# Kernel tuning notes

Hardware: AMD Instinct MI355X
Metric: run time of the kernel (lower is better)

## Reference

```python
import jax, jax.numpy as jnp
import numpy as np

HEADS = 8

def _flatten(x, s1, s2):
    # 'b c (h s1) (w s2) -> b (h w) (s1 s2 c)'
    b, c, H, W = x.shape
    h, w = H // s1, W // s2
    x = x.reshape(b, c, h, s1, w, s2).transpose(0, 2, 4, 3, 5, 1)
    return x.reshape(b, h * w, s1 * s2 * c)

def _unflatten(x, h, w, s1, s2):
    # 'b (h w) (s1 s2 c) -> b c (h s1) (w s2)'
    b, n, e = x.shape
    c = e // (s1 * s2)
    x = x.reshape(b, h, w, s1, s2, c).transpose(0, 5, 1, 3, 2, 4)
    return x.reshape(b, c, h * s1, w * s2)

def _attn(x_detail, x_context, wq, bq, wk, bk, wv, bv, wo, bo):
    E = x_detail.shape[-1]
    d = E // HEADS
    scale = d ** -0.5
    def split(t):
        b, n, _ = t.shape
        return t.reshape(b, n, HEADS, d).transpose(0, 2, 1, 3)  # b h n d
    q = split(x_context @ wq.T + bq)
    k = split(x_detail @ wk.T + bk)
    v = split(x_detail @ wv.T + bv)
    att = jax.nn.softmax(jnp.einsum('bhqd,bhkd->bhqk', q, k) * scale, axis=-1)
    out = jnp.einsum('bhqk,bhkd->bhqd', att, v)
    b, h, n, _ = out.shape
    out = out.transpose(0, 2, 1, 3).reshape(b, n, E)
    return out @ wo.T + bo

def setup_inputs() -> dict:
    key = jax.random.key(0)
    ks = iter(jax.random.split(key, 64))
    inp = {}
    xshapes = [(16, 96, 56, 56), (16, 192, 28, 28), (16, 384, 14, 14), (16, 768, 7, 7)]
    names = ['x00', 'x10', 'x20', 'x30']
    for nm, sh in zip(names, xshapes):
        inp[nm + '_detail'] = jax.random.normal(next(ks), sh, dtype=jnp.float32)
        inp[nm + '_context'] = jax.random.normal(next(ks), sh, dtype=jnp.float32)
    embs = [384, 192, 384, 768]
    for i, E in enumerate(embs):
        for p in ['q', 'k', 'v', 'o']:
            inp[f'w{p}{i}'] = jax.random.normal(next(ks), (E, E), dtype=jnp.float32) * 0.02
            inp[f'b{p}{i}'] = jnp.zeros((E,), dtype=jnp.float32)
    return inp

def reference(x00_detail, x00_context, x10_detail, x10_context,
              x20_detail, x20_context, x30_detail, x30_context,
              wq0, bq0, wk0, bk0, wv0, bv0, wo0, bo0,
              wq1, bq1, wk1, bk1, wv1, bv1, wo1, bo1,
              wq2, bq2, wk2, bk2, wv2, bv2, wo2, bo2,
              wq3, bq3, wk3, bk3, wv3, bv3, wo3, bo3):
    # scale 0: 56x56 with 2x2 patching -> 784 tokens, emb 384
    o0 = x00_detail + _unflatten(
        _attn(_flatten(x00_detail, 2, 2), _flatten(x00_context, 2, 2),
              wq0, bq0, wk0, bk0, wv0, bv0, wo0, bo0), 28, 28, 2, 2)
    # scale 1: 28x28 -> 784 tokens, emb 192
    o1 = x10_detail + _unflatten(
        _attn(_flatten(x10_detail, 1, 1), _flatten(x10_context, 1, 1),
              wq1, bq1, wk1, bk1, wv1, bv1, wo1, bo1), 28, 28, 1, 1)
    # scale 2: 14x14 -> 196 tokens, emb 384
    o2 = x20_detail + _unflatten(
        _attn(_flatten(x20_detail, 1, 1), _flatten(x20_context, 1, 1),
              wq2, bq2, wk2, bk2, wv2, bv2, wo2, bo2), 14, 14, 1, 1)
    # scale 3: 7x7 -> 49 tokens, emb 768
    o3 = x30_detail + _unflatten(
        _attn(_flatten(x30_detail, 1, 1), _flatten(x30_context, 1, 1),
              wq3, bq3, wk3, bk3, wv3, bv3, wo3, bo3), 7, 7, 1, 1)
    return (o0, o1, o2, o3)
```

## Files before the change

### kernel.cpp

```cpp
#include <hip/hip_runtime.h>
#include <hip/hip_bf16.h>
#include <cstdint>
#include <cstddef>
#include <cmath>

typedef unsigned short bf16u;
typedef float f32x4 __attribute__((ext_vector_type(4)));
typedef short frag8 __attribute__((ext_vector_type(8)));

typedef __attribute__((address_space(1))) uint32_t u32g;
typedef __attribute__((address_space(3))) uint32_t u32l;

__device__ __forceinline__ void async_cp16(const bf16u* g, bf16u* l) {
    __builtin_amdgcn_global_load_lds((u32g*)g, (u32l*)l, 16, 0, 0);
}

__device__ __forceinline__ bf16u f2bf(float f) {
    union { float f; uint32_t u; } v; v.f = f;
    uint32_t u = v.u;
    return (bf16u)((u + 0x7fffu + ((u >> 16) & 1u)) >> 16);
}

__device__ __forceinline__ uint32_t pk2bf(float a, float b) {
    __hip_bfloat162 h = __float22bfloat162_rn(make_float2(a, b));
    union { __hip_bfloat162 h; uint32_t u; } c; c.h = h; return c.u;
}

__device__ __forceinline__ int vperm(int n) {
    return (n & ~63) | ((n & 15) << 2) | ((n >> 4) & 3);
}

static constexpr int cN[4]   = {784, 784, 196, 49};
static constexpr int cE[4]   = {384, 192, 384, 768};
static constexpr int cM[4]   = {12544, 12544, 3136, 784};
static constexpr int cC[4]   = {96, 192, 384, 768};
static constexpr int cH[4]   = {56, 28, 14, 7};
static constexpr int cS[4]   = {2, 1, 1, 1};
static constexpr int cWt[4]  = {28, 28, 14, 7};

static constexpr size_t xoff[4] = {0, 4816896, 7225344, 8429568};
static constexpr size_t voff[4] = {0, 6815744, 10223616, 12320768};
static constexpr size_t woff[4] = {0, 589824, 737280, 1327104};

__device__ __constant__ float qsc[4] = {0.20823509f, 0.29448888f, 0.20823509f, 0.14724444f};

static constexpr int qStartQ[5] = {0, 294, 369, 411, 999};
static constexpr int oStart[5]  = {0,294,369,411,999};

static constexpr int fStart[9] = {0,4800,9600,12000,14400,15744,17088,17856,18624};
static constexpr int wCum[17]  = {0,72,144,216,288,306,324,342,360,432,504,576,648,936,1224,1512,1800};
static constexpr int fNtn[4] = {25, 25, 7, 2};
static constexpr int fNtc[4] = {3, 6, 12, 24};
static constexpr int fSp[4]  = {4, 1, 1, 1};

struct BiasP { const float* p[16]; };
struct PrepP { const float* x[8]; const float* w[16]; };
struct OunfP { const float* xd[4]; };

__global__ __launch_bounds__(256) void prep(PrepP pp, bf16u* __restrict__ Xd,
                                            bf16u* __restrict__ Xc, bf16u* __restrict__ Wb) {
    int blk = blockIdx.x, tid = threadIdx.x;
    if (blk < 18624) {
        __shared__ float tile[32][33];
        int seg = 0;
        while (seg < 7 && blk >= fStart[seg + 1]) seg++;
        int s = seg >> 1, which = seg & 1;
        int l = blk - fStart[seg];
        int ntn = fNtn[s], ntc = fNtc[s], sp = fSp[s];
        int nt = l % ntn; l /= ntn;
        int ctl = l % ntc; l /= ntc;
        int spi = l % sp; int b = l / sp;
        int sv = cS[s];
        int s1i = spi / sv, s2i = spi % sv;
        int C = cC[s], H = cH[s], Wd = cH[s], N = cN[s], E2 = cE[s], Wt = cWt[s];
        const float* x = pp.x[s * 2 + which];
        bf16u* dst = (which ? Xc : Xd) + xoff[s];
        int tx = tid & 31, ty = tid >> 5;
        int n0 = nt * 32, c0 = ctl * 32;
#pragma unroll
        for (int rr = 0; rr < 4; ++rr) {
            int c = c0 + rr * 8 + ty;
            int n = n0 + tx;
            if (n < N) {
                int hh = (n / Wt) * sv + s1i;
                int ww = (n % Wt) * sv + s2i;
                tile[rr * 8 + ty][tx] = x[((size_t)(b * C + c) * H + hh) * Wd + ww];
            }
        }
        __syncthreads();
        int ebase = (s1i * sv + s2i) * C + c0;
#pragma unroll
        for (int rr = 0; rr < 4; ++rr) {
            int n = n0 + rr * 8 + ty;
            if (n < N)
                dst[((size_t)b * N + n) * E2 + ebase + tx] = f2bf(tile[tx][rr * 8 + ty]);
        }
    } else {
        int wb = blk - 18624;
        int m2 = 0;
        while (m2 < 15 && wb >= wCum[m2 + 1]) m2++;
        int s = m2 >> 2, mi = m2 & 3;
        size_t e2 = (size_t)cE[s] * cE[s];
        size_t base = (size_t)(wb - wCum[m2]) * 2048 + tid * 8;
        const float* src = pp.w[m2];
        bf16u* dst = Wb + woff[s] + mi * e2 + base;
        float4 a = *(const float4*)(src + base);
        float4 c = *(const float4*)(src + base + 4);
        bf16u o[8] = {f2bf(a.x), f2bf(a.y), f2bf(a.z), f2bf(a.w),
                      f2bf(c.x), f2bf(c.y), f2bf(c.z), f2bf(c.w)};
        *(frag8*)dst = *(frag8*)o;
    }
}

template<int MODE, int NN, int DHt, int DHPt, int NJt>
__device__ __forceinline__ void gemm_tile128(const bf16u* __restrict__ A, const bf16u* __restrict__ W,
                                             const float* __restrict__ bias,
                                             int M, int E, int mTile, int eTile, float oscale,
                                             bf16u* __restrict__ outB,
                                             bf16u* sm) {
    bf16u* A0 = sm;
    bf16u* B0 = sm + 4096;
    bf16u* A1 = sm + 8192;
    bf16u* B1 = sm + 12288;
    int tid = threadIdx.x, wave = tid >> 6, lane = tid & 63;
    int mbase = mTile * 128, ebase = eTile * 128;
    int wm = (wave & 1) * 64, wn = (wave >> 1) * 64;
    f32x4 acc[4][4] = {};
    int srow = tid >> 2, sch = (tid & 3) * 8;
    int K = E;
    int m0 = mbase + srow;      if (m0 >= M) m0 = M - 1;
    int m1 = mbase + srow + 64; if (m1 >= M) m1 = M - 1;
    const bf16u* Ag0 = A + (size_t)m0 * K + sch;
    const bf16u* Ag1 = A + (size_t)m1 * K + sch;
    const bf16u* Wg0 = W + (size_t)(ebase + srow) * K + sch;
    const bf16u* Wg1 = W + (size_t)(ebase + srow + 64) * K + sch;
    int la = (lane & 15) * 32 + (lane >> 4) * 8;

    auto stage = [&](int k0, bf16u* As, bf16u* Bs) {
        async_cp16(Ag0 + k0, As + tid * 8);
        async_cp16(Ag1 + k0, As + 2048 + tid * 8);
        async_cp16(Wg0 + k0, Bs + tid * 8);
        async_cp16(Wg1 + k0, Bs + 2048 + tid * 8);
    };
    auto compute = [&](const bf16u* As, const bf16u* Bs) {
        frag8 af[4], bfr[4];
#pragma unroll
        for (int i = 0; i < 4; ++i) {
            af[i]  = *(const frag8*)(As + (wm + i * 16) * 32 + la);
            bfr[i] = *(const frag8*)(Bs + (wn + i * 16) * 32 + la);
        }
#pragma unroll
        for (int i = 0; i < 4; ++i)
#pragma unroll
            for (int j = 0; j < 4; ++j)
                acc[i][j] = __builtin_amdgcn_mfma_f32_16x16x32_bf16(af[i], bfr[j], acc[i][j], 0, 0, 0);
    };

    stage(0, A0, B0);
    __syncthreads();
    for (int k0 = 0; k0 < K; k0 += 64) {
        stage(k0 + 32, A1, B1);
        compute(A0, B0);
        __syncthreads();
        if (k0 + 64 < K) stage(k0 + 64, A0, B0);
        compute(A1, B1);
        if (k0 + 64 < K) __syncthreads();
    }

#pragma unroll
    for (int mt = 0; mt < 4; ++mt) {
#pragma unroll
        for (int nt = 0; nt < 4; ++nt) {
            int col = ebase + wn + nt * 16 + (lane & 15);
            float bv = bias[col];
            int rbase = mbase + wm + mt * 16 + (lane >> 4) * 4;
#pragma unroll
            for (int r = 0; r < 4; ++r) {
                int rowg = rbase + r;
                if (rowg >= M) continue;
                float val = (acc[mt][nt][r] + bv) * oscale;
                if (MODE == 0) {
                    outB[(size_t)rowg * E + col] = f2bf(val);
                } else {
                    int bb2 = rowg / NN, n = rowg % NN;
                    int hh = col / DHt, d = col - hh * DHt;
                    outB[((size_t)(bb2 * 8 + hh) * DHPt + d) * NJt + vperm(n)] = f2bf(val);
                }
            }
        }
    }
}

template<int MODE, int NN, int DHt, int DHPt, int NJt>
__device__ __forceinline__ void gemm_tile64(const bf16u* __restrict__ A, const bf16u* __restrict__ W,
                                            const float* __restrict__ bias,
                                            int M, int E, int mTile, int eTile, float oscale,
                                            bf16u* __restrict__ outB,
                                            bf16u* sm) {
    bf16u* A0 = sm;
    bf16u* B0 = sm + 2048;
    bf16u* A1 = sm + 4096;
    bf16u* B1 = sm + 6144;
    int tid = threadIdx.x, wave = tid >> 6, lane = tid & 63;
    int mbase = mTile * 64, ebase = eTile * 64;
    int wm = (wave & 1) * 32, wn = (wave >> 1) * 32;
    f32x4 acc[2][2] = {};
    int srow = tid >> 2, sch = (tid & 3) * 8;
    int K = E;
    int m = mbase + srow; if (m >= M) m = M - 1;
    const bf16u* Ag = A + (size_t)m * K + sch;
    const bf16u* Wg = W + (size_t)(ebase + srow) * K + sch;
    int la = (lane & 15) * 32 + (lane >> 4) * 8;

    auto stage = [&](int k0, bf16u* As, bf16u* Bs) {
        async_cp16(Ag + k0, As + tid * 8);
        async_cp16(Wg + k0, Bs + tid * 8);
    };
    auto compute = [&](const bf16u* As, const bf16u* Bs) {
        frag8 af0 = *(const frag8*)(As + wm * 32 + la);
        frag8 af1 = *(const frag8*)(As + (wm + 16) * 32 + la);
        frag8 bf0 = *(const frag8*)(Bs + wn * 32 + la);
        frag8 bf1 = *(const frag8*)(Bs + (wn + 16) * 32 + la);
        acc[0][0] = __builtin_amdgcn_mfma_f32_16x16x32_bf16(af0, bf0, acc[0][0], 0, 0, 0);
        acc[0][1] = __builtin_amdgcn_mfma_f32_16x16x32_bf16(af0, bf1, acc[0][1], 0, 0, 0);
        acc[1][0] = __builtin_amdgcn_mfma_f32_16x16x32_bf16(af1, bf0, acc[1][0], 0, 0, 0);
        acc[1][1] = __builtin_amdgcn_mfma_f32_16x16x32_bf16(af1, bf1, acc[1][1], 0, 0, 0);
    };

    stage(0, A0, B0);
    __syncthreads();
    for (int k0 = 0; k0 < K; k0 += 64) {
        stage(k0 + 32, A1, B1);
        compute(A0, B0);
        __syncthreads();
        if (k0 + 64 < K) stage(k0 + 64, A0, B0);
        compute(A1, B1);
        if (k0 + 64 < K) __syncthreads();
    }

#pragma unroll
    for (int mt = 0; mt < 2; ++mt) {
#pragma unroll
        for (int nt = 0; nt < 2; ++nt) {
            int col = ebase + wn + nt * 16 + (lane & 15);
            float bv = bias[col];
            int rbase = mbase + wm + mt * 16 + (lane >> 4) * 4;
#pragma unroll
            for (int r = 0; r < 4; ++r) {
                int rowg = rbase + r;
                if (rowg >= M) continue;
                float val = (acc[mt][nt][r] + bv) * oscale;
                if (MODE == 0) {
                    outB[(size_t)rowg * E + col] = f2bf(val);
                } else {
                    int bb2 = rowg / NN, n = rowg % NN;
                    int hh = col / DHt, d = col - hh * DHt;
                    outB[((size_t)(bb2 * 8 + hh) * DHPt + d) * NJt + vperm(n)] = f2bf(val);
                }
            }
        }
    }
}

template<int NN, int DHt, int DHPt, int NJt>
__device__ __forceinline__ void gemm_kv128(const bf16u* __restrict__ A, const bf16u* __restrict__ Wk,
                                           const bf16u* __restrict__ Wv,
                                           const float* __restrict__ bk, const float* __restrict__ bv,
                                           int M, int E, int mTile, int eTile,
                                           bf16u* __restrict__ Ko, bf16u* __restrict__ Vo, bf16u* sm) {
    bf16u* As = sm;
    bf16u* Ks = sm + 4096;
    bf16u* Vs = sm + 8192;
    int tid = threadIdx.x, wave = tid >> 6, lane = tid & 63;
    int mbase = mTile * 128, ebase = eTile * 128;
    int wm = (wave & 1) * 64, wn = (wave >> 1) * 64;
    f32x4 acck[4][4] = {};
    f32x4 accv[4][4] = {};
    int srow = tid >> 2, sch = (tid & 3) * 8;
    int Kd = E;
    int m0 = mbase + srow;      if (m0 >= M) m0 = M - 1;
    int m1 = mbase + srow + 64; if (m1 >= M) m1 = M - 1;
    const bf16u* Ag0 = A + (size_t)m0 * Kd + sch;
    const bf16u* Ag1 = A + (size_t)m1 * Kd + sch;
    const bf16u* Kg0 = Wk + (size_t)(ebase + srow) * Kd + sch;
    const bf16u* Kg1 = Wk + (size_t)(ebase + srow + 64) * Kd + sch;
    const bf16u* Vg0 = Wv + (size_t)(ebase + srow) * Kd + sch;
    const bf16u* Vg1 = Wv + (size_t)(ebase + srow + 64) * Kd + sch;
    int la = (lane & 15) * 32 + (lane >> 4) * 8;

    for (int k0 = 0; k0 < Kd; k0 += 32) {
        async_cp16(Ag0 + k0, As + tid * 8);
        async_cp16(Ag1 + k0, As + 2048 + tid * 8);
        async_cp16(Kg0 + k0, Ks + tid * 8);
        async_cp16(Kg1 + k0, Ks + 2048 + tid * 8);
        async_cp16(Vg0 + k0, Vs + tid * 8);
        async_cp16(Vg1 + k0, Vs + 2048 + tid * 8);
        __syncthreads();
        frag8 af[4], bfr[4];
#pragma unroll
        for (int i = 0; i < 4; ++i)
            af[i] = *(const frag8*)(As + (wm + i * 16) * 32 + la);
#pragma unroll
        for (int i = 0; i < 4; ++i)
            bfr[i] = *(const frag8*)(Ks + (wn + i * 16) * 32 + la);
#pragma unroll
        for (int i = 0; i < 4; ++i)
#pragma unroll
            for (int j = 0; j < 4; ++j)
                acck[i][j] = __builtin_amdgcn_mfma_f32_16x16x32_bf16(af[i], bfr[j], acck[i][j], 0, 0, 0);
#pragma unroll
        for (int i = 0; i < 4; ++i)
            bfr[i] = *(const frag8*)(Vs + (wn + i * 16) * 32 + la);
#pragma unroll
        for (int i = 0; i < 4; ++i)
#pragma unroll
            for (int j = 0; j < 4; ++j)
                accv[i][j] = __builtin_amdgcn_mfma_f32_16x16x32_bf16(af[i], bfr[j], accv[i][j], 0, 0, 0);
        __syncthreads();
    }

#pragma unroll
    for (int mt = 0; mt < 4; ++mt) {
#pragma unroll
        for (int nt = 0; nt < 4; ++nt) {
            int col = ebase + wn + nt * 16 + (lane & 15);
            float bkc = bk[col];
            float bvc = bv[col];
            int hh = col / DHt, d = col - hh * DHt;
            int rbase = mbase + wm + mt * 16 + (lane >> 4) * 4;
#pragma unroll
            for (int r = 0; r < 4; ++r) {
                int rowg = rbase + r;
                if (rowg >= M) continue;
                Ko[(size_t)rowg * E + col] = f2bf(acck[mt][nt][r] + bkc);
                int bb2 = rowg / NN, n = rowg % NN;
                Vo[((size_t)(bb2 * 8 + hh) * DHPt + d) * NJt + vperm(n)] = f2bf(accv[mt][nt][r] + bvc);
            }
        }
    }
}

template<int NN, int DHt, int DHPt, int NJt>
__device__ __forceinline__ void gemm_kv64(const bf16u* __restrict__ A, const bf16u* __restrict__ Wk,
                                          const bf16u* __restrict__ Wv,
                                          const float* __restrict__ bk, const float* __restrict__ bv,
                                          int M, int E, int mTile, int eTile,
                                          bf16u* __restrict__ Ko, bf16u* __restrict__ Vo, bf16u* sm) {
    bf16u* As = sm;
    bf16u* Ks = sm + 2048;
    bf16u* Vs = sm + 4096;
    int tid = threadIdx.x, wave = tid >> 6, lane = tid & 63;
    int mbase = mTile * 64, ebase = eTile * 64;
    int wm = (wave & 1) * 32, wn = (wave >> 1) * 32;
    f32x4 acck[2][2] = {};
    f32x4 accv[2][2] = {};
    int srow = tid >> 2, sch = (tid & 3) * 8;
    int Kd = E;
    int m = mbase + srow; if (m >= M) m = M - 1;
    const bf16u* Ag = A + (size_t)m * Kd + sch;
    const bf16u* Kg = Wk + (size_t)(ebase + srow) * Kd + sch;
    const bf16u* Vg = Wv + (size_t)(ebase + srow) * Kd + sch;
    int la = (lane & 15) * 32 + (lane >> 4) * 8;

    for (int k0 = 0; k0 < Kd; k0 += 32) {
        async_cp16(Ag + k0, As + tid * 8);
        async_cp16(Kg + k0, Ks + tid * 8);
        async_cp16(Vg + k0, Vs + tid * 8);
        __syncthreads();
        frag8 af0 = *(const frag8*)(As + wm * 32 + la);
        frag8 af1 = *(const frag8*)(As + (wm + 16) * 32 + la);
        frag8 k0f = *(const frag8*)(Ks + wn * 32 + la);
        frag8 k1f = *(const frag8*)(Ks + (wn + 16) * 32 + la);
        acck[0][0] = __builtin_amdgcn_mfma_f32_16x16x32_bf16(af0, k0f, acck[0][0], 0, 0, 0);
        acck[0][1] = __builtin_amdgcn_mfma_f32_16x16x32_bf16(af0, k1f, acck[0][1], 0, 0, 0);
        acck[1][0] = __builtin_amdgcn_mfma_f32_16x16x32_bf16(af1, k0f, acck[1][0], 0, 0, 0);
        acck[1][1] = __builtin_amdgcn_mfma_f32_16x16x32_bf16(af1, k1f, acck[1][1], 0, 0, 0);
        frag8 v0f = *(const frag8*)(Vs + wn * 32 + la);
        frag8 v1f = *(const frag8*)(Vs + (wn + 16) * 32 + la);
        accv[0][0] = __builtin_amdgcn_mfma_f32_16x16x32_bf16(af0, v0f, accv[0][0], 0, 0, 0);
        accv[0][1] = __builtin_amdgcn_mfma_f32_16x16x32_bf16(af0, v1f, accv[0][1], 0, 0, 0);
        accv[1][0] = __builtin_amdgcn_mfma_f32_16x16x32_bf16(af1, v0f, accv[1][0], 0, 0, 0);
        accv[1][1] = __builtin_amdgcn_mfma_f32_16x16x32_bf16(af1, v1f, accv[1][1], 0, 0, 0);
        __syncthreads();
    }

#pragma unroll
    for (int mt = 0; mt < 2; ++mt) {
#pragma unroll
        for (int nt = 0; nt < 2; ++nt) {
            int col = ebase + wn + nt * 16 + (lane & 15);
            float bkc = bk[col];
            float bvc = bv[col];
            int hh = col / DHt, d = col - hh * DHt;
            int rbase = mbase + wm + mt * 16 + (lane >> 4) * 4;
#pragma unroll
            for (int r = 0; r < 4; ++r) {
                int rowg = rbase + r;
                if (rowg >= M) continue;
                Ko[(size_t)rowg * E + col] = f2bf(acck[mt][nt][r] + bkc);
                int bb2 = rowg / NN, n = rowg % NN;
                Vo[((size_t)(bb2 * 8 + hh) * DHPt + d) * NJt + vperm(n)] = f2bf(accv[mt][nt][r] + bvc);
            }
        }
    }
}

__global__ __launch_bounds__(256, 2) void qkv_all(const bf16u* __restrict__ Xd, const bf16u* __restrict__ Xc,
                                                  const bf16u* __restrict__ Wb,
                                                  bf16u* __restrict__ Qb, bf16u* __restrict__ Kb,
                                                  bf16u* __restrict__ Vt, BiasP bp) {
    __shared__ __align__(16) bf16u sm[16384];
    int blk0 = blockIdx.x;
    if (blk0 < 999) {
        int blk = blk0;
        int seg = 0;
        while (seg < 3 && blk >= qStartQ[seg + 1]) seg++;
        int t = blk - qStartQ[seg];
        if (seg < 3) {
            int s = (seg == 0) ? 0 : (seg == 1 ? 2 : 3);
            int E = cE[s], M = cM[s];
            int ct = E >> 7;
            int mTile = t / ct, eTile = t - mTile * ct;
            const bf16u* A  = Xd + xoff[s];
            const bf16u* Wk = Wb + woff[s] + (size_t)1 * E * E;
            const bf16u* Wv = Wb + woff[s] + (size_t)2 * E * E;
            if (s == 0)
                gemm_kv128<784, 48, 64, 832>(A, Wk, Wv, bp.p[1], bp.p[2], M, E, mTile, eTile,
                                             Kb + xoff[0], Vt + voff[0], sm);
            else if (s == 2)
                gemm_kv128<196, 48, 64, 256>(A, Wk, Wv, bp.p[9], bp.p[10], M, E, mTile, eTile,
                                             Kb + xoff[2], Vt + voff[2], sm);
            else
                gemm_kv128<49, 96, 96, 64>(A, Wk, Wv, bp.p[13], bp.p[14], M, E, mTile, eTile,
                                           Kb + xoff[3], Vt + voff[3], sm);
        } else {
            int E = 192, M = 12544;
            int mTile = t / 3, eTile = t - mTile * 3;
            gemm_kv64<784, 24, 32, 832>(Xd + xoff[1], Wb + woff[1] + (size_t)1 * E * E,
                                        Wb + woff[1] + (size_t)2 * E * E, bp.p[5], bp.p[6],
                                        M, E, mTile, eTile, Kb + xoff[1], Vt + voff[1], sm);
        }
    } else {
        int blk = blk0 - 999;
        int seg = 0;
        while (seg < 3 && blk >= qStartQ[seg + 1]) seg++;
        int t = blk - qStartQ[seg];
        if (seg < 3) {
            int s = (seg == 0) ? 0 : (seg == 1 ? 2 : 3);
            int E = cE[s], M = cM[s];
            int ct = E >> 7;
            int mTile = t / ct, eTile = t - mTile * ct;
            gemm_tile128<0, 0, 1, 0, 0>(Xc + xoff[s], Wb + woff[s], bp.p[s * 4], M, E, mTile, eTile,
                                        qsc[s], Qb + xoff[s], sm);
        } else {
            int E = 192, M = 12544;
            int mTile = t / 3, eTile = t - mTile * 3;
            gemm_tile64<0, 0, 1, 0, 0>(Xc + xoff[1], Wb + woff[1], bp.p[4], M, E, mTile, eTile,
                                       qsc[1], Qb + xoff[1], sm);
        }
    }
}

__device__ __forceinline__ f32x4 bfly_add16(f32x4 v) {
#pragma unroll
    for (int m = 1; m <= 8; m <<= 1) {
        f32x4 o;
#pragma unroll
        for (int e = 0; e < 4; ++e) o[e] = __shfl_xor(v[e], m);
#pragma unroll
        for (int e = 0; e < 4; ++e) v[e] += o[e];
    }
    return v;
}

template<int DH, int N>
__device__ __forceinline__ void attn_body3(bf16u* __restrict__ smem,
                                           const bf16u* __restrict__ Q, const bf16u* __restrict__ K,
                                           const bf16u* __restrict__ Vt, bf16u* __restrict__ O,
                                           int lin) {
    constexpr int DHP = (DH == 24) ? 32 : 64;
    constexpr int C8  = DHP / 8;
    constexpr int CM  = C8 - 1;
    constexpr int KC  = DHP / 32;
    constexpr int DHT = (DH + 15) / 16;
    constexpr int VR  = DHT * 16;
    constexpr int NT  = (N + 63) / 64;
    constexpr int QT  = (N + 127) / 128;
    constexpr int NJc = NT * 64;
    constexpr int E   = DH * 8;
    constexpr int KS  = 64 * C8;
    constexpr int TS  = KS + VR * 8;
    constexpr int RND = (TS + 255) / 256;
    constexpr int PP  = 72;

    bf16u* buf0 = smem;
    bf16u* buf1 = smem + (size_t)TS * 8;
    bf16u* Ps   = smem + (size_t)2 * TS * 8;

    const int qt = lin % QT;
    const int r2 = lin / QT;
    const int h = r2 & 7, b = r2 >> 3;
    const int qb = qt * 128;
    const int tid = threadIdx.x, wave = tid >> 6, lane = tid & 63;
    const int mrow = lane & 15, quad = lane >> 4;

    const bf16u* Kb2 = K + (size_t)b * N * E + h * DH;
    const bf16u* Vb2 = Vt + (size_t)(b * 8 + h) * DHP * NJc;

    auto stage = [&](int jt, bf16u* buf) {
#pragma unroll
        for (int r = 0; r < RND; ++r) {
            int s = tid + r * 256;
            bf16u* dst = buf + (size_t)s * 8;
            if (s < KS) {
                int row = s / C8;
                int cl = (s & CM) ^ (row & CM);
                int n = jt * 64 + row; if (n >= N) n = N - 1;
                async_cp16(Kb2 + (size_t)n * E + cl * 8, dst);
            } else if (s < TS) {
                int v = s - KS;
                int d = v >> 3;
                int cl = (v & 7) ^ (d & 7);
                async_cp16(Vb2 + (size_t)d * NJc + jt * 64 + cl * 8, dst);
            }
        }
    };

    stage(0, buf0);

    frag8 qf0[KC], qf1[KC];
    {
        int qn0 = qb + wave * 32 + mrow;      if (qn0 >= N) qn0 = N - 1;
        int qn1 = qb + wave * 32 + 16 + mrow; if (qn1 >= N) qn1 = N - 1;
        const bf16u* qp0 = Q + (size_t)(b * N + qn0) * E + h * DH;
        const bf16u* qp1 = Q + (size_t)(b * N + qn1) * E + h * DH;
#pragma unroll
        for (int kc = 0; kc < KC; ++kc) {
            int col = kc * 32 + quad * 8;
            frag8 v0 = {}, v1 = {};
            if (col < DH) { v0 = *(const frag8*)(qp0 + col); v1 = *(const frag8*)(qp1 + col); }
            qf0[kc] = v0; qf1[kc] = v1;
        }
    }

    f32x4 lrun0 = {0.f, 0.f, 0.f, 0.f};
    f32x4 lrun1 = {0.f, 0.f, 0.f, 0.f};
    f32x4 oacc0[DHT], oacc1[DHT];
#pragma unroll
    for (int t = 0; t < DHT; ++t) { oacc0[t] = f32x4{0.f,0.f,0.f,0.f}; oacc1[t] = f32x4{0.f,0.f,0.f,0.f}; }

    bf16u* Pw = Ps + wave * 32 * PP;

    __syncthreads();

    int p = 0;
    for (int jt = 0; jt < NT; ++jt) {
        bf16u* KsB = p ? buf1 : buf0;
        bf16u* VsB = KsB + (size_t)KS * 8;
        if (jt + 1 < NT) stage(jt + 1, p ? buf0 : buf1);

        f32x4 s0[4], s1[4];
        const bool domask = ((N & 63) != 0) && (jt == NT - 1);
#pragma unroll
        for (int sub = 0; sub < 4; ++sub) {
            f32x4 a0 = {}, a1 = {};
#pragma unroll
            for (int kc = 0; kc < KC; ++kc) {
                int c = kc * 4 + quad;
                frag8 bfr = *(const frag8*)(KsB + ((size_t)((sub * 16 + mrow) * C8 + (c ^ (mrow & CM)))) * 8);
                a0 = __builtin_amdgcn_mfma_f32_16x16x32_bf16(qf0[kc], bfr, a0, 0, 0, 0);
                a1 = __builtin_amdgcn_mfma_f32_16x16x32_bf16(qf1[kc], bfr, a1, 0, 0, 0);
            }
            if (domask) {
                int col = jt * 64 + sub * 16 + mrow;
                if (col >= N) {
                    a0[0] = a0[1] = a0[2] = a0[3] = -30000.f;
                    a1[0] = a1[1] = a1[2] = a1[3] = -30000.f;
                }
            }
            s0[sub] = a0; s1[sub] = a1;
        }

#pragma unroll
        for (int sub = 0; sub < 4; ++sub)
#pragma unroll
            for (int e = 0; e < 4; ++e) {
                float p0 = __builtin_amdgcn_exp2f(s0[sub][e]);
                float p1 = __builtin_amdgcn_exp2f(s1[sub][e]);
                s0[sub][e] = p0; s1[sub][e] = p1;
                lrun0[e] += p0; lrun1[e] += p1;
            }

#pragma unroll
        for (int e = 0; e < 4; ++e) {
            uint2 u0, u1;
            u0.x = pk2bf(s0[0][e], s0[1][e]);
            u0.y = pk2bf(s0[2][e], s0[3][e]);
            u1.x = pk2bf(s1[0][e], s1[1][e]);
            u1.y = pk2bf(s1[2][e], s1[3][e]);
            *(uint2*)(Pw + (quad * 4 + e) * PP + mrow * 4) = u0;
            *(uint2*)(Pw + (16 + quad * 4 + e) * PP + mrow * 4) = u1;
        }

#pragma unroll
        for (int jc = 0; jc < 2; ++jc) {
            frag8 af0 = *(const frag8*)(Pw + mrow * PP + jc * 32 + quad * 8);
            frag8 af1 = *(const frag8*)(Pw + (16 + mrow) * PP + jc * 32 + quad * 8);
            int c = jc * 4 + quad;
#pragma unroll
            for (int t = 0; t < DHT; ++t) {
                frag8 bfr = *(const frag8*)(VsB + ((size_t)((t * 16 + mrow) * 8 + (c ^ (mrow & 7)))) * 8);
                oacc0[t] = __builtin_amdgcn_mfma_f32_16x16x32_bf16(af0, bfr, oacc0[t], 0, 0, 0);
                oacc1[t] = __builtin_amdgcn_mfma_f32_16x16x32_bf16(af1, bfr, oacc1[t], 0, 0, 0);
            }
        }
        __syncthreads();
        p ^= 1;
    }

    lrun0 = bfly_add16(lrun0);
    lrun1 = bfly_add16(lrun1);
    f32x4 linv0, linv1;
#pragma unroll
    for (int e = 0; e < 4; ++e) { linv0[e] = 1.0f / lrun0[e]; linv1[e] = 1.0f / lrun1[e]; }
#pragma unroll
    for (int t = 0; t < DHT; ++t) {
        int d = t * 16 + mrow;
        if (d >= DH) continue;
#pragma unroll
        for (int e = 0; e < 4; ++e) {
            int n0 = qb + wave * 32 + quad * 4 + e;
            int n1 = n0 + 16;
            if (n0 < N)
                O[((size_t)(b * N + n0)) * E + h * DH + d] = f2bf(oacc0[t][e] * linv0[e]);
            if (n1 < N)
                O[((size_t)(b * N + n1)) * E + h * DH + d] = f2bf(oacc1[t][e] * linv1[e]);
        }
    }
}

__device__ __forceinline__ void attn_s3_body(bf16u* __restrict__ smem,
                                             const bf16u* __restrict__ Qg, const bf16u* __restrict__ Kg,
                                             const bf16u* __restrict__ Vtg, bf16u* __restrict__ Og,
                                             int lin) {
    constexpr int DH = 96, N = 49, DHP = 96, KC = 3, DHT = 6, NJc = 64, E = 768;
    constexpr int KP = 104, QP = 104, VP = 72, PP = 72, C8 = 12;
    bf16u* Ks = smem;
    bf16u* Vs = Ks + 64 * KP;
    bf16u* QsPw = Vs + DHT * 16 * VP;

    const bf16u* Q = Qg + xoff[3];
    const bf16u* K = Kg + xoff[3];
    const bf16u* Vt = Vtg + voff[3];
    bf16u* O = Og + xoff[3];

    int h = lin & 7, b = lin >> 3;
    int tid = threadIdx.x, wave = tid >> 6, lane = tid & 63;
    int mrow = lane & 15, quad = lane >> 4;

    for (int idx = tid; idx < 64 * C8; idx += 256) {
        int row = idx / C8, col = (idx % C8) * 8;
        int n = row; if (n >= N) n = N - 1;
        frag8 v = {};
        if (col < DH) v = *(const frag8*)(Q + ((size_t)(b * N + n)) * E + h * DH + col);
        *(frag8*)(QsPw + row * QP + col) = v;
    }
    for (int idx = tid; idx < 64 * C8; idx += 256) {
        int row = idx / C8, col = (idx % C8) * 8;
        int n = row; if (n >= N) n = N - 1;
        frag8 v = {};
        if (col < DH) v = *(const frag8*)(K + (size_t)(b * N + n) * E + h * DH + col);
        *(frag8*)(Ks + row * KP + col) = v;
    }
    const bf16u* Vb2 = Vt + (size_t)(b * 8 + h) * DHP * NJc;
    for (int idx = tid; idx < DHT * 16 * 8; idx += 256) {
        int d = idx / 8, j = (idx % 8) * 8;
        frag8 v = {};
        if (d < DH) v = *(const frag8*)(Vb2 + (size_t)d * NJc + j);
        *(frag8*)(Vs + d * VP + j) = v;
    }
    __syncthreads();
    frag8 qf[KC];
#pragma unroll
    for (int kc = 0; kc < KC; ++kc)
        qf[kc] = *(const frag8*)(QsPw + (wave * 16 + mrow) * QP + kc * 32 + quad * 8);
    __syncthreads();
    bf16u* Pw = QsPw + wave * 16 * PP;

    f32x4 lrun = {0.f, 0.f, 0.f, 0.f};
    f32x4 oacc[DHT];
#pragma unroll
    for (int t = 0; t < DHT; ++t) oacc[t] = f32x4{0.f, 0.f, 0.f, 0.f};

    f32x4 s[4];
#pragma unroll
    for (int sub = 0; sub < 4; ++sub) {
        f32x4 acc = {};
#pragma unroll
        for (int kc = 0; kc < KC; ++kc) {
            frag8 bfr = *(const frag8*)(Ks + (sub * 16 + mrow) * KP + kc * 32 + quad * 8);
            acc = __builtin_amdgcn_mfma_f32_16x16x32_bf16(qf[kc], bfr, acc, 0, 0, 0);
        }
        int col = sub * 16 + mrow;
        if (col >= N) { acc[0] = acc[1] = acc[2] = acc[3] = -30000.f; }
        s[sub] = acc;
    }
#pragma unroll
    for (int sub = 0; sub < 4; ++sub)
#pragma unroll
        for (int e = 0; e < 4; ++e) {
            float px = __builtin_amdgcn_exp2f(s[sub][e]);
            s[sub][e] = px;
            lrun[e] += px;
        }
#pragma unroll
    for (int e = 0; e < 4; ++e) {
        uint2 u;
        u.x = pk2bf(s[0][e], s[1][e]);
        u.y = pk2bf(s[2][e], s[3][e]);
        *(uint2*)(Pw + (quad * 4 + e) * PP + mrow * 4) = u;
    }
#pragma unroll
    for (int jc = 0; jc < 2; ++jc) {
        frag8 af = *(const frag8*)(Pw + mrow * PP + jc * 32 + quad * 8);
#pragma unroll
        for (int t = 0; t < DHT; ++t) {
            frag8 bfr = *(const frag8*)(Vs + (t * 16 + mrow) * VP + jc * 32 + quad * 8);
            oacc[t] = __builtin_amdgcn_mfma_f32_16x16x32_bf16(af, bfr, oacc[t], 0, 0, 0);
        }
    }

    lrun = bfly_add16(lrun);
    f32x4 linv;
#pragma unroll
    for (int e = 0; e < 4; ++e) linv[e] = 1.0f / lrun[e];
#pragma unroll
    for (int t = 0; t < DHT; ++t) {
        int d = t * 16 + mrow;
#pragma unroll
        for (int e = 0; e < 4; ++e) {
            int n = wave * 16 + quad * 4 + e;
            if (n < N)
                O[((size_t)(b * N + n)) * E + h * DH + d] = f2bf(oacc[t][e] * linv[e]);
        }
    }
}

__global__ __launch_bounds__(256, 3) void attn_all(const bf16u* __restrict__ Qb, const bf16u* __restrict__ Kb,
                                                   const bf16u* __restrict__ Vt, bf16u* __restrict__ Ob) {
    __shared__ __align__(16) bf16u smem[23552];
    int g = blockIdx.x;
    if (g < 896) {
        int l = (g & 7) * 112 + (g >> 3);
        attn_body3<48, 784>(smem, Qb + xoff[0], Kb + xoff[0], Vt + voff[0], Ob + xoff[0], l);
    } else if (g < 1792) {
        int gg = g - 896;
        int l = (gg & 7) * 112 + (gg >> 3);
        attn_body3<24, 784>(smem, Qb + xoff[1], Kb + xoff[1], Vt + voff[1], Ob + xoff[1], l);
    } else if (g < 2048) {
        int gg = g - 1792;
        int l = (gg & 7) * 32 + (gg >> 3);
        attn_body3<48, 196>(smem, Qb + xoff[2], Kb + xoff[2], Vt + voff[2], Ob + xoff[2], l);
    } else {
        attn_s3_body(smem, Qb, Kb, Vt, Ob, g - 2048);
    }
}

template<int SC>
__device__ __forceinline__ size_t out_index(int rowg, int cg) {
    if (SC == 0) {
        int b = rowg / 784, n = rowg - b * 784;
        int slot = cg / 96, c = cg - slot * 96;
        int hh = n / 28, ww = n - hh * 28;
        return ((size_t)(b * 96 + c) * 56 + 2 * hh + (slot >> 1)) * 56 + 2 * ww + (slot & 1);
    } else if (SC == 1) {
        int b = rowg / 784, n = rowg - b * 784;
        return ((size_t)(b * 192 + cg)) * 784 + n;
    } else if (SC == 2) {
        int b = rowg / 196, n = rowg - b * 196;
        return ((size_t)(b * 384 + cg)) * 196 + n;
    } else {
        int b = rowg / 49, n = rowg - b * 49;
        return ((size_t)(b * 768 + cg)) * 49 + n;
    }
}

template<int SC>
__device__ __forceinline__ void o_tile128(const bf16u* __restrict__ A, const bf16u* __restrict__ W,
                                          const float* __restrict__ bias,
                                          const float* __restrict__ xd, float* __restrict__ out,
                                          int M, int E, int mTile, int eTile, bf16u* sm) {
    bf16u* A0 = sm;
    bf16u* B0 = sm + 4096;
    bf16u* A1 = sm + 8192;
    bf16u* B1 = sm + 12288;
    int tid = threadIdx.x, wave = tid >> 6, lane = tid & 63;
    int mbase = mTile * 128, ebase = eTile * 128;
    int wm = (wave & 1) * 64, wn = (wave >> 1) * 64;
    int mrow = lane & 15, quad = lane >> 4;
    f32x4 acc[4][4] = {};
    int srow = tid >> 2, sch = (tid & 3) * 8;
    int K = E;
    int m0 = mbase + srow;      if (m0 >= M) m0 = M - 1;
    int m1 = mbase + srow + 64; if (m1 >= M) m1 = M - 1;
    const bf16u* Ag0 = A + (size_t)m0 * K + sch;
    const bf16u* Ag1 = A + (size_t)m1 * K + sch;
    const bf16u* Wg0 = W + (size_t)(ebase + srow) * K + sch;
    const bf16u* Wg1 = W + (size_t)(ebase + srow + 64) * K + sch;
    int la = mrow * 32 + quad * 8;

    auto stage = [&](int k0, bf16u* As, bf16u* Bs) {
        async_cp16(Ag0 + k0, As + tid * 8);
        async_cp16(Ag1 + k0, As + 2048 + tid * 8);
        async_cp16(Wg0 + k0, Bs + tid * 8);
        async_cp16(Wg1 + k0, Bs + 2048 + tid * 8);
    };
    auto compute = [&](const bf16u* As, const bf16u* Bs) {
        frag8 af[4], bfr[4];
#pragma unroll
        for (int i = 0; i < 4; ++i) {
            af[i]  = *(const frag8*)(As + (wm + i * 16) * 32 + la);
            bfr[i] = *(const frag8*)(Bs + (wn + i * 16) * 32 + la);
        }
#pragma unroll
        for (int i = 0; i < 4; ++i)
#pragma unroll
            for (int j = 0; j < 4; ++j)
                acc[i][j] = __builtin_amdgcn_mfma_f32_16x16x32_bf16(af[i], bfr[j], acc[i][j], 0, 0, 0);
    };

    stage(0, A0, B0);
    __syncthreads();
    for (int k0 = 0; k0 < K; k0 += 64) {
        stage(k0 + 32, A1, B1);
        compute(A0, B0);
        __syncthreads();
        if (k0 + 64 < K) stage(k0 + 64, A0, B0);
        compute(A1, B1);
        if (k0 + 64 < K) __syncthreads();
    }

    float* Ls = (float*)sm;
#pragma unroll
    for (int ph = 0; ph < 4; ++ph) {
        __syncthreads();
        if ((wave & 1) == (ph >> 1)) {
            int mt0 = (ph & 1) * 2;
#pragma unroll
            for (int mi = 0; mi < 2; ++mi) {
                int mt = mt0 + mi;
#pragma unroll
                for (int nt = 0; nt < 4; ++nt)
#pragma unroll
                    for (int r = 0; r < 4; ++r)
                        Ls[(mi * 16 + quad * 4 + r) * 133 + wn + nt * 16 + mrow] = acc[mt][nt][r];
            }
        }
        __syncthreads();
        int rb = mbase + ph * 32;
#pragma unroll
        for (int i = 0; i < 16; ++i) {
            int coll = (tid >> 5) + i * 8;
            int l = tid & 31;
            int rg = rb + l;
            if (rg < M) {
                int cg = ebase + coll;
                size_t oi = out_index<SC>(rg, cg);
                out[oi] = xd[oi] + Ls[l * 133 + coll] + bias[cg];
            }
        }
    }
}

__device__ __forceinline__ void o_tile64_s1(const bf16u* __restrict__ A, const bf16u* __restrict__ W,
                                            const float* __restrict__ bias,
                                            const float* __restrict__ xd, float* __restrict__ out,
                                            int M, int E, int mTile, int eTile, bf16u* sm) {
    bf16u* A0 = sm;
    bf16u* B0 = sm + 2048;
    bf16u* A1 = sm + 4096;
    bf16u* B1 = sm + 6144;
    int tid = threadIdx.x, wave = tid >> 6, lane = tid & 63;
    int mbase = mTile * 64, ebase = eTile * 64;
    int wm = (wave & 1) * 32, wn = (wave >> 1) * 32;
    int mrow = lane & 15, quad = lane >> 4;
    f32x4 acc[2][2] = {};
    int srow = tid >> 2, sch = (tid & 3) * 8;
    int K = E;
    int m = mbase + srow; if (m >= M) m = M - 1;
    const bf16u* Ag = A + (size_t)m * K + sch;
    const bf16u* Wg = W + (size_t)(ebase + srow) * K + sch;
    int la = mrow * 32 + quad * 8;

    auto stage = [&](int k0, bf16u* As, bf16u* Bs) {
        async_cp16(Ag + k0, As + tid * 8);
        async_cp16(Wg + k0, Bs + tid * 8);
    };
    auto compute = [&](const bf16u* As, const bf16u* Bs) {
        frag8 af0 = *(const frag8*)(As + wm * 32 + la);
        frag8 af1 = *(const frag8*)(As + (wm + 16) * 32 + la);
        frag8 bf0 = *(const frag8*)(Bs + wn * 32 + la);
        frag8 bf1 = *(const frag8*)(Bs + (wn + 16) * 32 + la);
        acc[0][0] = __builtin_amdgcn_mfma_f32_16x16x32_bf16(af0, bf0, acc[0][0], 0, 0, 0);
        acc[0][1] = __builtin_amdgcn_mfma_f32_16x16x32_bf16(af0, bf1, acc[0][1], 0, 0, 0);
        acc[1][0] = __builtin_amdgcn_mfma_f32_16x16x32_bf16(af1, bf0, acc[1][0], 0, 0, 0);
        acc[1][1] = __builtin_amdgcn_mfma_f32_16x16x32_bf16(af1, bf1, acc[1][1], 0, 0, 0);
    };

    stage(0, A0, B0);
    __syncthreads();
    for (int k0 = 0; k0 < K; k0 += 64) {
        stage(k0 + 32, A1, B1);
        compute(A0, B0);
        __syncthreads();
        if (k0 + 64 < K) stage(k0 + 64, A0, B0);
        compute(A1, B1);
        if (k0 + 64 < K) __syncthreads();
    }

    float* Ls = (float*)sm;
#pragma unroll
    for (int ph = 0; ph < 2; ++ph) {
        __syncthreads();
        if ((wave & 1) == ph) {
#pragma unroll
            for (int mt = 0; mt < 2; ++mt)
#pragma unroll
                for (int nt = 0; nt < 2; ++nt)
#pragma unroll
                    for (int r = 0; r < 4; ++r)
                        Ls[(mt * 16 + quad * 4 + r) * 69 + wn + nt * 16 + mrow] = acc[mt][nt][r];
        }
        __syncthreads();
        int rb = mbase + ph * 32;
#pragma unroll
        for (int i = 0; i < 8; ++i) {
            int coll = (tid >> 5) + i * 8;
            int l = tid & 31;
            int rg = rb + l;
            if (rg < M) {
                int cg = ebase + coll;
                size_t oi = out_index<1>(rg, cg);
                out[oi] = xd[oi] + Ls[l * 69 + coll] + bias[cg];
            }
        }
    }
}

__global__ __launch_bounds__(256) void ounf_fat(const bf16u* __restrict__ Ob, const bf16u* __restrict__ Wb,
                                                float* __restrict__ out, BiasP bp, OunfP up) {
    __shared__ __align__(16) bf16u sm[16384];
    int blk = blockIdx.x;
    int seg = 0;
    while (seg < 3 && blk >= oStart[seg + 1]) seg++;
    int t = blk - oStart[seg];
    if (seg < 3) {
        int s = (seg == 0) ? 0 : (seg == 1 ? 2 : 3);
        int E = cE[s], M = cM[s];
        int ct = E >> 7;
        int mTile = t / ct, eTile = t - mTile * ct;
        const bf16u* A = Ob + xoff[s];
        const bf16u* W = Wb + woff[s] + (size_t)3 * E * E;
        if (s == 0)
            o_tile128<0>(A, W, bp.p[3], up.xd[0], out + xoff[0], M, E, mTile, eTile, sm);
        else if (s == 2)
            o_tile128<2>(A, W, bp.p[11], up.xd[2], out + xoff[2], M, E, mTile, eTile, sm);
        else
            o_tile128<3>(A, W, bp.p[15], up.xd[3], out + xoff[3], M, E, mTile, eTile, sm);
    } else {
        int E = 192, M = 12544;
        int mTile = t / 3, eTile = t - mTile * 3;
        o_tile64_s1(Ob + xoff[1], Wb + woff[1] + (size_t)3 * E * E, bp.p[7],
                    up.xd[1], out + xoff[1], M, E, mTile, eTile, sm);
    }
}

extern "C" void kernel_launch(void* const* d_in, const int* in_sizes, int n_in,
                              void* d_out, int out_size, void* d_ws, size_t ws_size,
                              hipStream_t stream) {
    bf16u* ws = (bf16u*)d_ws;
    bf16u* Qb = ws;
    bf16u* Kb = ws + 9031680;
    bf16u* Vt = ws + 18063360;
    bf16u* Ob = ws + 31170560;
    bf16u* Wb = ws + 40202240;
    bf16u* Xd = ws + 43888640;
    bf16u* Xc = ws + 52920320;
    float* out = (float*)d_out;

    PrepP pp; BiasP bb; OunfP ux;
    for (int s = 0; s < 4; ++s) {
        pp.x[s * 2]     = (const float*)d_in[s * 2];
        pp.x[s * 2 + 1] = (const float*)d_in[s * 2 + 1];
        ux.xd[s]        = (const float*)d_in[s * 2];
        int w0 = 8 + s * 8;
        pp.w[s * 4 + 0] = (const float*)d_in[w0 + 0];
        pp.w[s * 4 + 1] = (const float*)d_in[w0 + 2];
        pp.w[s * 4 + 2] = (const float*)d_in[w0 + 4];
        pp.w[s * 4 + 3] = (const float*)d_in[w0 + 6];
        bb.p[s * 4 + 0] = (const float*)d_in[w0 + 1];
        bb.p[s * 4 + 1] = (const float*)d_in[w0 + 3];
        bb.p[s * 4 + 2] = (const float*)d_in[w0 + 5];
        bb.p[s * 4 + 3] = (const float*)d_in[w0 + 7];
    }

    prep<<<20424, 256, 0, stream>>>(pp, Xd, Xc, Wb);
    qkv_all<<<1998, 256, 0, stream>>>(Xd, Xc, Wb, Qb, Kb, Vt, bb);
    attn_all<<<2176, 256, 0, stream>>>(Qb, Kb, Vt, Ob);
    ounf_fat<<<999, 256, 0, stream>>>(Ob, Wb, out, bb, ux);
}
```

Measured before the change: 363.3 us.

## Triple-buffer GEMM tiles with explicit vmcnt waits and raw barriers

```diff
diff --git a/kernel.cpp b/kernel.cpp
--- a/kernel.cpp
+++ b/kernel.cpp
@@ -28,6 +28,21 @@
 
 __device__ __forceinline__ int vperm(int n) {
     return (n & ~63) | ((n & 15) << 2) | ((n >> 4) & 3);
+}
+
+template<int N> __device__ __forceinline__ void vmw() {
+    if constexpr (N == 0)  asm volatile("s_waitcnt vmcnt(0)" ::: "memory");
+    if constexpr (N == 2)  asm volatile("s_waitcnt vmcnt(2)" ::: "memory");
+    if constexpr (N == 3)  asm volatile("s_waitcnt vmcnt(3)" ::: "memory");
+    if constexpr (N == 4)  asm volatile("s_waitcnt vmcnt(4)" ::: "memory");
+    if constexpr (N == 6)  asm volatile("s_waitcnt vmcnt(6)" ::: "memory");
+    if constexpr (N == 8)  asm volatile("s_waitcnt vmcnt(8)" ::: "memory");
+    if constexpr (N == 12) asm volatile("s_waitcnt vmcnt(12)" ::: "memory");
+}
+__device__ __forceinline__ void xbar() {
+    __builtin_amdgcn_sched_barrier(0);
+    __builtin_amdgcn_s_barrier();
+    __builtin_amdgcn_sched_barrier(0);
 }
 
 static constexpr int cN[4]   = {784, 784, 196, 49};
@@ -118,10 +133,6 @@
                                              int M, int E, int mTile, int eTile, float oscale,
                                              bf16u* __restrict__ outB,
                                              bf16u* sm) {
-    bf16u* A0 = sm;
-    bf16u* B0 = sm + 4096;
-    bf16u* A1 = sm + 8192;
-    bf16u* B1 = sm + 12288;
     int tid = threadIdx.x, wave = tid >> 6, lane = tid & 63;
     int mbase = mTile * 128, ebase = eTile * 128;
     int wm = (wave & 1) * 64, wn = (wave >> 1) * 64;
@@ -136,13 +147,15 @@
     const bf16u* Wg1 = W + (size_t)(ebase + srow + 64) * K + sch;
     int la = (lane & 15) * 32 + (lane >> 4) * 8;
 
-    auto stage = [&](int k0, bf16u* As, bf16u* Bs) {
-        async_cp16(Ag0 + k0, As + tid * 8);
-        async_cp16(Ag1 + k0, As + 2048 + tid * 8);
-        async_cp16(Wg0 + k0, Bs + tid * 8);
-        async_cp16(Wg1 + k0, Bs + 2048 + tid * 8);
-    };
-    auto compute = [&](const bf16u* As, const bf16u* Bs) {
+    auto stage = [&](int k0, bf16u* buf) {
+        async_cp16(Ag0 + k0, buf + tid * 8);
+        async_cp16(Ag1 + k0, buf + 2048 + tid * 8);
+        async_cp16(Wg0 + k0, buf + 4096 + tid * 8);
+        async_cp16(Wg1 + k0, buf + 6144 + tid * 8);
+    };
+    auto compute = [&](const bf16u* buf) {
+        const bf16u* As = buf;
+        const bf16u* Bs = buf + 4096;
         frag8 af[4], bfr[4];
 #pragma unroll
         for (int i = 0; i < 4; ++i) {
@@ -156,15 +169,24 @@
                 acc[i][j] = __builtin_amdgcn_mfma_f32_16x16x32_bf16(af[i], bfr[j], acc[i][j], 0, 0, 0);
     };
 
-    stage(0, A0, B0);
-    __syncthreads();
-    for (int k0 = 0; k0 < K; k0 += 64) {
-        stage(k0 + 32, A1, B1);
-        compute(A0, B0);
-        __syncthreads();
-        if (k0 + 64 < K) stage(k0 + 64, A0, B0);
-        compute(A1, B1);
-        if (k0 + 64 < K) __syncthreads();
+    bf16u* B0 = sm;
+    bf16u* B1 = sm + 8192;
+    bf16u* B2 = sm + 16384;
+    stage(0, B0);
+    stage(32, B1);
+    for (int k0 = 0; k0 < K; k0 += 96) {
+        stage(k0 + 64, B2);
+        vmw<8>(); xbar();
+        compute(B0);
+        xbar();
+        if (k0 + 96 < K) { stage(k0 + 96, B0); vmw<8>(); } else vmw<4>();
+        xbar();
+        compute(B1);
+        xbar();
+        if (k0 + 128 < K) { stage(k0 + 128, B1); vmw<8>(); } else vmw<0>();
+        xbar();
+        compute(B2);
+        xbar();
     }
 
 #pragma unroll
@@ -197,10 +219,6 @@
                                             int M, int E, int mTile, int eTile, float oscale,
                                             bf16u* __restrict__ outB,
                                             bf16u* sm) {
-    bf16u* A0 = sm;
-    bf16u* B0 = sm + 2048;
-    bf16u* A1 = sm + 4096;
-    bf16u* B1 = sm + 6144;
     int tid = threadIdx.x, wave = tid >> 6, lane = tid & 63;
     int mbase = mTile * 64, ebase = eTile * 64;
     int wm = (wave & 1) * 32, wn = (wave >> 1) * 32;
@@ -212,11 +230,13 @@
     const bf16u* Wg = W + (size_t)(ebase + srow) * K + sch;
     int la = (lane & 15) * 32 + (lane >> 4) * 8;
 
-    auto stage = [&](int k0, bf16u* As, bf16u* Bs) {
-        async_cp16(Ag + k0, As + tid * 8);
-        async_cp16(Wg + k0, Bs + tid * 8);
-    };
-    auto compute = [&](const bf16u* As, const bf16u* Bs) {
+    auto stage = [&](int k0, bf16u* buf) {
+        async_cp16(Ag + k0, buf + tid * 8);
+        async_cp16(Wg + k0, buf + 2048 + tid * 8);
+    };
+    auto compute = [&](const bf16u* buf) {
+        const bf16u* As = buf;
+        const bf16u* Bs = buf + 2048;
         frag8 af0 = *(const frag8*)(As + wm * 32 + la);
         frag8 af1 = *(const frag8*)(As + (wm + 16) * 32 + la);
         frag8 bf0 = *(const frag8*)(Bs + wn * 32 + la);
@@ -227,15 +247,24 @@
         acc[1][1] = __builtin_amdgcn_mfma_f32_16x16x32_bf16(af1, bf1, acc[1][1], 0, 0, 0);
     };
 
-    stage(0, A0, B0);
-    __syncthreads();
-    for (int k0 = 0; k0 < K; k0 += 64) {
-        stage(k0 + 32, A1, B1);
-        compute(A0, B0);
-        __syncthreads();
-        if (k0 + 64 < K) stage(k0 + 64, A0, B0);
-        compute(A1, B1);
-        if (k0 + 64 < K) __syncthreads();
+    bf16u* B0 = sm;
+    bf16u* B1 = sm + 4096;
+    bf16u* B2 = sm + 8192;
+    stage(0, B0);
+    stage(32, B1);
+    for (int k0 = 0; k0 < K; k0 += 96) {
+        stage(k0 + 64, B2);
+        vmw<4>(); xbar();
+        compute(B0);
+        xbar();
+        if (k0 + 96 < K) { stage(k0 + 96, B0); vmw<4>(); } else vmw<2>();
+        xbar();
+        compute(B1);
+        xbar();
+        if (k0 + 128 < K) { stage(k0 + 128, B1); vmw<4>(); } else vmw<0>();
+        xbar();
+        compute(B2);
+        xbar();
     }
 
 #pragma unroll
@@ -268,9 +297,6 @@
                                            const float* __restrict__ bk, const float* __restrict__ bv,
                                            int M, int E, int mTile, int eTile,
                                            bf16u* __restrict__ Ko, bf16u* __restrict__ Vo, bf16u* sm) {
-    bf16u* As = sm;
-    bf16u* Ks = sm + 4096;
-    bf16u* Vs = sm + 8192;
     int tid = threadIdx.x, wave = tid >> 6, lane = tid & 63;
     int mbase = mTile * 128, ebase = eTile * 128;
     int wm = (wave & 1) * 64, wn = (wave >> 1) * 64;
@@ -288,14 +314,18 @@
     const bf16u* Vg1 = Wv + (size_t)(ebase + srow + 64) * Kd + sch;
     int la = (lane & 15) * 32 + (lane >> 4) * 8;
 
-    for (int k0 = 0; k0 < Kd; k0 += 32) {
-        async_cp16(Ag0 + k0, As + tid * 8);
-        async_cp16(Ag1 + k0, As + 2048 + tid * 8);
-        async_cp16(Kg0 + k0, Ks + tid * 8);
-        async_cp16(Kg1 + k0, Ks + 2048 + tid * 8);
-        async_cp16(Vg0 + k0, Vs + tid * 8);
-        async_cp16(Vg1 + k0, Vs + 2048 + tid * 8);
-        __syncthreads();
+    auto stage = [&](int k0, bf16u* buf) {
+        async_cp16(Ag0 + k0, buf + tid * 8);
+        async_cp16(Ag1 + k0, buf + 2048 + tid * 8);
+        async_cp16(Kg0 + k0, buf + 4096 + tid * 8);
+        async_cp16(Kg1 + k0, buf + 6144 + tid * 8);
+        async_cp16(Vg0 + k0, buf + 8192 + tid * 8);
+        async_cp16(Vg1 + k0, buf + 10240 + tid * 8);
+    };
+    auto compute = [&](const bf16u* buf) {
+        const bf16u* As = buf;
+        const bf16u* Ks = buf + 4096;
+        const bf16u* Vs = buf + 8192;
         frag8 af[4], bfr[4];
 #pragma unroll
         for (int i = 0; i < 4; ++i)
@@ -316,7 +346,26 @@
 #pragma unroll
             for (int j = 0; j < 4; ++j)
                 accv[i][j] = __builtin_amdgcn_mfma_f32_16x16x32_bf16(af[i], bfr[j], accv[i][j], 0, 0, 0);
-        __syncthreads();
+    };
+
+    bf16u* B0 = sm;
+    bf16u* B1 = sm + 12288;
+    bf16u* B2 = sm + 24576;
+    stage(0, B0);
+    stage(32, B1);
+    for (int k0 = 0; k0 < Kd; k0 += 96) {
+        stage(k0 + 64, B2);
+        vmw<12>(); xbar();
+        compute(B0);
+        xbar();
+        if (k0 + 96 < Kd) { stage(k0 + 96, B0); vmw<12>(); } else vmw<6>();
+        xbar();
+        compute(B1);
+        xbar();
+        if (k0 + 128 < Kd) { stage(k0 + 128, B1); vmw<12>(); } else vmw<0>();
+        xbar();
+        compute(B2);
+        xbar();
     }
 
 #pragma unroll
@@ -346,9 +395,6 @@
                                           const float* __restrict__ bk, const float* __restrict__ bv,
                                           int M, int E, int mTile, int eTile,
                                           bf16u* __restrict__ Ko, bf16u* __restrict__ Vo, bf16u* sm) {
-    bf16u* As = sm;
-    bf16u* Ks = sm + 2048;
-    bf16u* Vs = sm + 4096;
     int tid = threadIdx.x, wave = tid >> 6, lane = tid & 63;
     int mbase = mTile * 64, ebase = eTile * 64;
     int wm = (wave & 1) * 32, wn = (wave >> 1) * 32;
@@ -362,11 +408,15 @@
     const bf16u* Vg = Wv + (size_t)(ebase + srow) * Kd + sch;
     int la = (lane & 15) * 32 + (lane >> 4) * 8;
 
-    for (int k0 = 0; k0 < Kd; k0 += 32) {
-        async_cp16(Ag + k0, As + tid * 8);
-        async_cp16(Kg + k0, Ks + tid * 8);
-        async_cp16(Vg + k0, Vs + tid * 8);
-        __syncthreads();
+    auto stage = [&](int k0, bf16u* buf) {
+        async_cp16(Ag + k0, buf + tid * 8);
+        async_cp16(Kg + k0, buf + 2048 + tid * 8);
+        async_cp16(Vg + k0, buf + 4096 + tid * 8);
+    };
+    auto compute = [&](const bf16u* buf) {
+        const bf16u* As = buf;
+        const bf16u* Ks = buf + 2048;
+        const bf16u* Vs = buf + 4096;
         frag8 af0 = *(const frag8*)(As + wm * 32 + la);
         frag8 af1 = *(const frag8*)(As + (wm + 16) * 32 + la);
         frag8 k0f = *(const frag8*)(Ks + wn * 32 + la);
@@ -381,7 +431,26 @@
         accv[0][1] = __builtin_amdgcn_mfma_f32_16x16x32_bf16(af0, v1f, accv[0][1], 0, 0, 0);
         accv[1][0] = __builtin_amdgcn_mfma_f32_16x16x32_bf16(af1, v0f, accv[1][0], 0, 0, 0);
         accv[1][1] = __builtin_amdgcn_mfma_f32_16x16x32_bf16(af1, v1f, accv[1][1], 0, 0, 0);
-        __syncthreads();
+    };
+
+    bf16u* B0 = sm;
+    bf16u* B1 = sm + 6144;
+    bf16u* B2 = sm + 12288;
+    stage(0, B0);
+    stage(32, B1);
+    for (int k0 = 0; k0 < Kd; k0 += 96) {
+        stage(k0 + 64, B2);
+        vmw<6>(); xbar();
+        compute(B0);
+        xbar();
+        if (k0 + 96 < Kd) { stage(k0 + 96, B0); vmw<6>(); } else vmw<3>();
+        xbar();
+        compute(B1);
+        xbar();
+        if (k0 + 128 < Kd) { stage(k0 + 128, B1); vmw<6>(); } else vmw<0>();
+        xbar();
+        compute(B2);
+        xbar();
     }
 
 #pragma unroll
@@ -409,7 +478,7 @@
                                                   const bf16u* __restrict__ Wb,
                                                   bf16u* __restrict__ Qb, bf16u* __restrict__ Kb,
                                                   bf16u* __restrict__ Vt, BiasP bp) {
-    __shared__ __align__(16) bf16u sm[16384];
+    __shared__ __align__(16) bf16u sm[36864];
     int blk0 = blockIdx.x;
     if (blk0 < 999) {
         int blk = blk0;
@@ -790,10 +859,6 @@
                                           const float* __restrict__ bias,
                                           const float* __restrict__ xd, float* __restrict__ out,
                                           int M, int E, int mTile, int eTile, bf16u* sm) {
-    bf16u* A0 = sm;
-    bf16u* B0 = sm + 4096;
-    bf16u* A1 = sm + 8192;
-    bf16u* B1 = sm + 12288;
     int tid = threadIdx.x, wave = tid >> 6, lane = tid & 63;
     int mbase = mTile * 128, ebase = eTile * 128;
     int wm = (wave & 1) * 64, wn = (wave >> 1) * 64;
@@ -809,13 +874,15 @@
     const bf16u* Wg1 = W + (size_t)(ebase + srow + 64) * K + sch;
     int la = mrow * 32 + quad * 8;
 
-    auto stage = [&](int k0, bf16u* As, bf16u* Bs) {
-        async_cp16(Ag0 + k0, As + tid * 8);
-        async_cp16(Ag1 + k0, As + 2048 + tid * 8);
-        async_cp16(Wg0 + k0, Bs + tid * 8);
-        async_cp16(Wg1 + k0, Bs + 2048 + tid * 8);
-    };
-    auto compute = [&](const bf16u* As, const bf16u* Bs) {
+    auto stage = [&](int k0, bf16u* buf) {
+        async_cp16(Ag0 + k0, buf + tid * 8);
+        async_cp16(Ag1 + k0, buf + 2048 + tid * 8);
+        async_cp16(Wg0 + k0, buf + 4096 + tid * 8);
+        async_cp16(Wg1 + k0, buf + 6144 + tid * 8);
+    };
+    auto compute = [&](const bf16u* buf) {
+        const bf16u* As = buf;
+        const bf16u* Bs = buf + 4096;
         frag8 af[4], bfr[4];
 #pragma unroll
         for (int i = 0; i < 4; ++i) {
@@ -829,15 +896,24 @@
                 acc[i][j] = __builtin_amdgcn_mfma_f32_16x16x32_bf16(af[i], bfr[j], acc[i][j], 0, 0, 0);
     };
 
-    stage(0, A0, B0);
-    __syncthreads();
-    for (int k0 = 0; k0 < K; k0 += 64) {
-        stage(k0 + 32, A1, B1);
-        compute(A0, B0);
-        __syncthreads();
-        if (k0 + 64 < K) stage(k0 + 64, A0, B0);
-        compute(A1, B1);
-        if (k0 + 64 < K) __syncthreads();
+    bf16u* B0 = sm;
+    bf16u* B1 = sm + 8192;
+    bf16u* B2 = sm + 16384;
+    stage(0, B0);
+    stage(32, B1);
+    for (int k0 = 0; k0 < K; k0 += 96) {
+        stage(k0 + 64, B2);
+        vmw<8>(); xbar();
+        compute(B0);
+        xbar();
+        if (k0 + 96 < K) { stage(k0 + 96, B0); vmw<8>(); } else vmw<4>();
+        xbar();
+        compute(B1);
+        xbar();
+        if (k0 + 128 < K) { stage(k0 + 128, B1); vmw<8>(); } else vmw<0>();
+        xbar();
+        compute(B2);
+        xbar();
     }
 
     float* Ls = (float*)sm;
@@ -876,10 +952,6 @@
                                             const float* __restrict__ bias,
                                             const float* __restrict__ xd, float* __restrict__ out,
                                             int M, int E, int mTile, int eTile, bf16u* sm) {
-    bf16u* A0 = sm;
-    bf16u* B0 = sm + 2048;
-    bf16u* A1 = sm + 4096;
-    bf16u* B1 = sm + 6144;
     int tid = threadIdx.x, wave = tid >> 6, lane = tid & 63;
     int mbase = mTile * 64, ebase = eTile * 64;
     int wm = (wave & 1) * 32, wn = (wave >> 1) * 32;
@@ -892,11 +964,13 @@
     const bf16u* Wg = W + (size_t)(ebase + srow) * K + sch;
     int la = mrow * 32 + quad * 8;
 
-    auto stage = [&](int k0, bf16u* As, bf16u* Bs) {
-        async_cp16(Ag + k0, As + tid * 8);
-        async_cp16(Wg + k0, Bs + tid * 8);
-    };
-    auto compute = [&](const bf16u* As, const bf16u* Bs) {
+    auto stage = [&](int k0, bf16u* buf) {
+        async_cp16(Ag + k0, buf + tid * 8);
+        async_cp16(Wg + k0, buf + 2048 + tid * 8);
+    };
+    auto compute = [&](const bf16u* buf) {
+        const bf16u* As = buf;
+        const bf16u* Bs = buf + 2048;
         frag8 af0 = *(const frag8*)(As + wm * 32 + la);
         frag8 af1 = *(const frag8*)(As + (wm + 16) * 32 + la);
         frag8 bf0 = *(const frag8*)(Bs + wn * 32 + la);
@@ -907,15 +981,24 @@
         acc[1][1] = __builtin_amdgcn_mfma_f32_16x16x32_bf16(af1, bf1, acc[1][1], 0, 0, 0);
     };
 
-    stage(0, A0, B0);
-    __syncthreads();
-    for (int k0 = 0; k0 < K; k0 += 64) {
-        stage(k0 + 32, A1, B1);
-        compute(A0, B0);
-        __syncthreads();
-        if (k0 + 64 < K) stage(k0 + 64, A0, B0);
-        compute(A1, B1);
-        if (k0 + 64 < K) __syncthreads();
+    bf16u* B0 = sm;
+    bf16u* B1 = sm + 4096;
+    bf16u* B2 = sm + 8192;
+    stage(0, B0);
+    stage(32, B1);
+    for (int k0 = 0; k0 < K; k0 += 96) {
+        stage(k0 + 64, B2);
+        vmw<4>(); xbar();
+        compute(B0);
+        xbar();
+        if (k0 + 96 < K) { stage(k0 + 96, B0); vmw<4>(); } else vmw<2>();
+        xbar();
+        compute(B1);
+        xbar();
+        if (k0 + 128 < K) { stage(k0 + 128, B1); vmw<4>(); } else vmw<0>();
+        xbar();
+        compute(B2);
+        xbar();
     }
 
     float* Ls = (float*)sm;
@@ -949,7 +1032,7 @@
 
 __global__ __launch_bounds__(256) void ounf_fat(const bf16u* __restrict__ Ob, const bf16u* __restrict__ Wb,
                                                 float* __restrict__ out, BiasP bp, OunfP up) {
-    __shared__ __align__(16) bf16u sm[16384];
+    __shared__ __align__(16) bf16u sm[24576];
     int blk = blockIdx.x;
     int seg = 0;
     while (seg < 3 && blk >= oStart[seg + 1]) seg++;
```

Result: no change. 361.6 us (-0.5%).
